# Performance work log

Measured on AMD Instinct MI355X. Metric: run time of the kernel, lower is better.

Reference implementation:

```python
import jax, jax.numpy as jnp
import numpy as np

B, MAX_T, S, H, NB, NA = 64, 511, 1024, 4096, 8, 4


def setup_inputs() -> dict:
    key = jax.random.key(0)
    k1, k2, k3, k4, k5 = jax.random.split(key, 5)
    s_i_batch = jax.random.normal(k1, (B, MAX_T + 1, S), dtype=jnp.float32)
    actions_batch = jax.random.randint(k2, (B, MAX_T), 0, NA, dtype=jnp.int32)
    lengths = jax.random.randint(k3, (B,), 0, MAX_T, dtype=jnp.int32)
    W1 = jax.random.normal(k4, (S, H), dtype=jnp.float32) * (1.0 / np.sqrt(S))
    b1 = jnp.zeros((H,), dtype=jnp.float32)
    W2 = jax.random.normal(k5, (H, NB * NA), dtype=jnp.float32) * (1.0 / np.sqrt(H))
    b2 = jnp.zeros((NB * NA,), dtype=jnp.float32)
    return {"s_i_batch": s_i_batch, "actions_batch": actions_batch,
            "lengths": lengths, "W1": W1, "b1": b1, "W2": W2, "b2": b2}


def reference(s_i_batch, actions_batch, lengths, W1, b1, W2, b2):
    Bc, Tp1, _ = s_i_batch.shape
    maxT = Tp1 - 1
    # control_net: MLP -> per-(option, action) log-probs
    h = jax.nn.relu(jnp.einsum('bts,sh->bth', s_i_batch, W1) + b1)
    logits = (jnp.einsum('bth,ha->bta', h, W2) + b2).reshape(Bc, Tp1, NB, NA)
    action_logps = jax.nn.log_softmax(logits, axis=-1)  # (B, T+1, b, 4)
    # option 0, timesteps 0..max_T-1
    lp0 = action_logps[:, :maxT, 0, :]                  # (B, max_T, 4)
    gathered = jnp.take_along_axis(lp0, actions_batch[..., None].astype(jnp.int32), axis=-1)[..., 0]
    mask = (jnp.arange(maxT)[None, :] < lengths[:, None]).astype(lp0.dtype)  # (B, max_T)
    total_logp = jnp.sum(gathered * mask)
    return -total_logp
```

## Files before the change

### kernel.cpp

```cpp
#include <hip/hip_runtime.h>
#include <hip/hip_bf16.h>
#include <math.h>

#define B_    64
#define MAXT  511
#define TP1   512
#define S_    1024
#define H_    4096
#define M_TOTAL (B_*TP1)
#define NITER (S_/32)

typedef __attribute__((ext_vector_type(8))) short  short8;
typedef __attribute__((ext_vector_type(4))) float  float4v;

#define ZBUF_BYTES ((size_t)M_TOTAL*4*sizeof(float))
#define SBF_OFF    0x81000
#define SBF_BYTES  ((size_t)M_TOTAL*S_*2)
#define W1T_OFF    (SBF_OFF + SBF_BYTES)

static __device__ __forceinline__ unsigned short f2bf(float f) {
    unsigned int u = __float_as_uint(f);
    u = u + 0x7fffu + ((u >> 16) & 1u);
    return (unsigned short)(u >> 16);
}

__global__ __launch_bounds__(256) void prep_kernel(const float* __restrict__ s,
                                                   const float* __restrict__ W1,
                                                   const int*   __restrict__ lengths,
                                                   unsigned short* __restrict__ Sb,
                                                   unsigned short* __restrict__ W1T) {
    int bid = blockIdx.x;
    if (bid < 16384) {
        int row = 2 * bid + (threadIdx.x >> 7);
        int b = row >> 9, t = row & 511;
        if (t >= lengths[b]) return;
        size_t idx = (size_t)row * S_ + (threadIdx.x & 127) * 8;
        float4v f0 = __builtin_nontemporal_load((const float4v*)(s + idx));
        float4v f1 = __builtin_nontemporal_load((const float4v*)(s + idx + 4));
        short8 o;
        o[0] = (short)f2bf(f0[0]); o[1] = (short)f2bf(f0[1]);
        o[2] = (short)f2bf(f0[2]); o[3] = (short)f2bf(f0[3]);
        o[4] = (short)f2bf(f1[0]); o[5] = (short)f2bf(f1[1]);
        o[6] = (short)f2bf(f1[2]); o[7] = (short)f2bf(f1[3]);
        *(short8*)(Sb + idx) = o;
    } else {
        __shared__ float tile[32][33];
        int tb = bid - 16384;
        int h0 = (tb & 127) * 32;
        int k0 = (tb >> 7) * 32;
        int tx = threadIdx.x & 31, ty = threadIdx.x >> 5;
        for (int r = ty; r < 32; r += 8)
            tile[r][tx] = __builtin_nontemporal_load(&W1[(size_t)(k0 + r) * H_ + h0 + tx]);
        __syncthreads();
        for (int r = ty; r < 32; r += 8)
            W1T[(size_t)(h0 + r) * S_ + k0 + tx] = f2bf(tile[tx][r]);
    }
}

__global__ __launch_bounds__(256) void gemm_fused_kernel(
        const unsigned short* __restrict__ Sb,
        const unsigned short* __restrict__ W1T,
        const float* __restrict__ b1,
        const float* __restrict__ W2,
        const int*   __restrict__ lengths,
        float*       __restrict__ zbuf)
{
    int id   = blockIdx.x;
    int xcd  = id & 7;
    int slot = id >> 3;
    int ntile = xcd * 4 + (slot & 3);
    int mtile = slot >> 2;

    int b  = mtile >> 2;
    int t0 = (mtile & 3) * 128;
    if (lengths[b] <= t0) return;

    int m0 = mtile * 128;
    int n0 = ntile * 128;

    __shared__ unsigned short smemA[2 * 128 * 32];
    __shared__ unsigned short smemB[2 * 128 * 32];

    int tid  = threadIdx.x;
    int wid  = tid >> 6;
    int lane = tid & 63;
    int lane15 = lane & 15;
    int quad   = lane >> 4;
    int wave_m = (wid >> 1) * 64;
    int wave_n = (wid & 1) * 64;

    int cA0 = tid, cA1 = tid + 256;
    int mA0 = cA0 >> 2, cp0 = cA0 & 3, q0 = cp0 ^ ((mA0 >> 1) & 3);
    int mA1 = cA1 >> 2, cp1 = cA1 & 3, q1 = cp1 ^ ((mA1 >> 1) & 3);

    const char* gA0 = (const char*)Sb  + (size_t)(m0 + mA0) * (S_*2) + q0 * 16;
    const char* gA1 = (const char*)Sb  + (size_t)(m0 + mA1) * (S_*2) + q1 * 16;
    const char* gB0 = (const char*)W1T + (size_t)(n0 + mA0) * (S_*2) + q0 * 16;
    const char* gB1 = (const char*)W1T + (size_t)(n0 + mA1) * (S_*2) + q1 * 16;
    char* lwA0 = (char*)smemA + cA0 * 16;
    char* lwA1 = (char*)smemA + cA1 * 16;
    char* lwB0 = (char*)smemB + cA0 * 16;
    char* lwB1 = (char*)smemB + cA1 * 16;

    int aOff[4], bOff[4];
#pragma unroll
    for (int s = 0; s < 4; s++) {
        int ml = wave_m + s * 16 + lane15;
        aOff[s] = ml * 32 + (quad ^ ((ml >> 1) & 3)) * 8;
        int nl = wave_n + s * 16 + lane15;
        bOff[s] = nl * 32 + (quad ^ ((nl >> 1) & 3)) * 8;
    }

    float4v acc[4][4] = {};
    short8 rA0[2], rA1[2], rB0[2], rB1[2];

    rA0[0] = *(const short8*)gA0; rA1[0] = *(const short8*)gA1;
    rB0[0] = *(const short8*)gB0; rB1[0] = *(const short8*)gB1;
    gA0 += 64; gA1 += 64; gB0 += 64; gB1 += 64;
    *(short8*)lwA0 = rA0[0]; *(short8*)lwA1 = rA1[0];
    *(short8*)lwB0 = rB0[0]; *(short8*)lwB1 = rB1[0];
    rA0[1] = *(const short8*)gA0; rA1[1] = *(const short8*)gA1;
    rB0[1] = *(const short8*)gB0; rB1[1] = *(const short8*)gB1;
    gA0 += 64; gA1 += 64; gB0 += 64; gB1 += 64;

    for (int k = 0; k < NITER; k += 2) {
        __syncthreads();
        if (k + 2 < NITER) {
            rA0[0] = *(const short8*)gA0; rA1[0] = *(const short8*)gA1;
            rB0[0] = *(const short8*)gB0; rB1[0] = *(const short8*)gB1;
            gA0 += 64; gA1 += 64; gB0 += 64; gB1 += 64;
        }
        *(short8*)(lwA0 + 8192) = rA0[1]; *(short8*)(lwA1 + 8192) = rA1[1];
        *(short8*)(lwB0 + 8192) = rB0[1]; *(short8*)(lwB1 + 8192) = rB1[1];
        {
            const unsigned short* aP = smemA;
            const unsigned short* bP = smemB;
            short8 af[4], bf[4];
#pragma unroll
            for (int s = 0; s < 4; s++) {
                af[s] = *(const short8*)(aP + aOff[s]);
                bf[s] = *(const short8*)(bP + bOff[s]);
            }
#pragma unroll
            for (int i = 0; i < 4; i++)
#pragma unroll
                for (int j = 0; j < 4; j++)
                    acc[i][j] = __builtin_amdgcn_mfma_f32_16x16x32_bf16(af[i], bf[j], acc[i][j], 0, 0, 0);
        }
        __syncthreads();
        if (k + 3 < NITER) {
            rA0[1] = *(const short8*)gA0; rA1[1] = *(const short8*)gA1;
            rB0[1] = *(const short8*)gB0; rB1[1] = *(const short8*)gB1;
            gA0 += 64; gA1 += 64; gB0 += 64; gB1 += 64;
        }
        if (k + 2 < NITER) {
            *(short8*)lwA0 = rA0[0]; *(short8*)lwA1 = rA1[0];
            *(short8*)lwB0 = rB0[0]; *(short8*)lwB1 = rB1[0];
        }
        {
            const unsigned short* aP = smemA + 4096;
            const unsigned short* bP = smemB + 4096;
            short8 af[4], bf[4];
#pragma unroll
            for (int s = 0; s < 4; s++) {
                af[s] = *(const short8*)(aP + aOff[s]);
                bf[s] = *(const short8*)(bP + bOff[s]);
            }
#pragma unroll
            for (int i = 0; i < 4; i++)
#pragma unroll
                for (int j = 0; j < 4; j++)
                    acc[i][j] = __builtin_amdgcn_mfma_f32_16x16x32_bf16(af[i], bf[j], acc[i][j], 0, 0, 0);
        }
    }

    float4v w2r[4];
    float   b1v[4];
#pragma unroll
    for (int ns = 0; ns < 4; ns++) {
        int n_g = n0 + wave_n + ns * 16 + lane15;
        w2r[ns] = *(const float4v*)(W2 + (size_t)n_g * 32);
        b1v[ns] = b1[n_g];
    }
#pragma unroll
    for (int ms = 0; ms < 4; ms++) {
        float p[4][4];
#pragma unroll
        for (int r = 0; r < 4; r++)
#pragma unroll
            for (int c = 0; c < 4; c++) p[r][c] = 0.f;
#pragma unroll
        for (int ns = 0; ns < 4; ns++) {
            float4v av = acc[ms][ns];
#pragma unroll
            for (int r = 0; r < 4; r++) {
                float h = av[r] + b1v[ns];
                h = h > 0.f ? h : 0.f;
                p[r][0] += h * w2r[ns][0];
                p[r][1] += h * w2r[ns][1];
                p[r][2] += h * w2r[ns][2];
                p[r][3] += h * w2r[ns][3];
            }
        }
#pragma unroll
        for (int off = 1; off < 16; off <<= 1)
#pragma unroll
            for (int r = 0; r < 4; r++)
#pragma unroll
                for (int c = 0; c < 4; c++)
                    p[r][c] += __shfl_xor(p[r][c], off);
        if (lane15 < 4) {
            int c = lane15;
#pragma unroll
            for (int r = 0; r < 4; r++) {
                int mg = m0 + wave_m + ms * 16 + quad * 4 + r;
                atomicAdd(&zbuf[(size_t)mg * 4 + c], p[r][c]);
            }
        }
    }
}

__global__ __launch_bounds__(128) void reduce_logp_kernel(
        const float* __restrict__ zbuf,
        const int*   __restrict__ actions,
        const int*   __restrict__ lengths,
        const float* __restrict__ b2,
        float*       __restrict__ out)
{
    int b = blockIdx.x;
    int t = blockIdx.y * 128 + threadIdx.x;
    int len = lengths[b];
    float local = 0.f;
    if (t < MAXT && t < len) {
        int row = b * TP1 + t;
        float4v z = *(const float4v*)(zbuf + (size_t)row * 4);
        float z0 = z[0] + b2[0], z1 = z[1] + b2[1], z2 = z[2] + b2[2], z3 = z[3] + b2[3];
        float mx = fmaxf(fmaxf(z0, z1), fmaxf(z2, z3));
        float se = expf(z0 - mx) + expf(z1 - mx) + expf(z2 - mx) + expf(z3 - mx);
        int a = actions[b * MAXT + t];
        float za = (a == 0) ? z0 : (a == 1) ? z1 : (a == 2) ? z2 : z3;
        local = (za - mx) - logf(se);
    }
#pragma unroll
    for (int off = 32; off > 0; off >>= 1) local += __shfl_xor(local, off);
    __shared__ float wsum[2];
    if ((threadIdx.x & 63) == 0) wsum[threadIdx.x >> 6] = local;
    __syncthreads();
    if (threadIdx.x == 0) atomicAdd(out, -(wsum[0] + wsum[1]));
}

extern "C" void kernel_launch(void* const* d_in, const int* in_sizes, int n_in,
                              void* d_out, int out_size, void* d_ws, size_t ws_size,
                              hipStream_t stream) {
    const float* s       = (const float*)d_in[0];
    const int*   actions = (const int*)  d_in[1];
    const int*   lengths = (const int*)  d_in[2];
    const float* W1      = (const float*)d_in[3];
    const float* b1      = (const float*)d_in[4];
    const float* W2      = (const float*)d_in[5];
    const float* b2      = (const float*)d_in[6];

    char* ws = (char*)d_ws;
    float*          zbuf = (float*)ws;
    unsigned short* Sb   = (unsigned short*)(ws + SBF_OFF);
    unsigned short* W1T  = (unsigned short*)(ws + W1T_OFF);

    hipMemsetAsync(ws, 0, ZBUF_BYTES, stream);
    hipMemsetAsync(d_out, 0, sizeof(float), stream);

    prep_kernel<<<dim3(16384 + 4096), 256, 0, stream>>>(s, W1, lengths, Sb, W1T);
    gemm_fused_kernel<<<dim3(8192), 256, 0, stream>>>(Sb, W1T, b1, W2, lengths, zbuf);
    reduce_logp_kernel<<<dim3(B_, 4), 128, 0, stream>>>(zbuf, actions, lengths, b2, (float*)d_out);
}
```

Before: 525.6 us.

## Use 512-thread GEMM blocks with 8 waves and widen W1 transpose tiles

The fused GEMM kernel moves from 4 waves with 64x64 tiles each to 8 waves with 64x32 tiles each over the same 128x128 block tile. Each thread now loads one 16-byte chunk per operand per stage, which cuts per-thread registers and raises the number of waves that can hide latency, at the cost of more LDS fragment reads per MFMA. The W1 transpose in the prep kernel switches to 64x64 tiles with float4 loads and 4-element bf16 stores, reducing block count and making memory accesses wider. The epilogue cross-lane reduction and the atomic updates now run across twice as many waves.

```diff
diff --git a/kernel.cpp b/kernel.cpp
--- a/kernel.cpp
+++ b/kernel.cpp
@@ -11,6 +11,7 @@
 #define NITER (S_/32)
 
 typedef __attribute__((ext_vector_type(8))) short  short8;
+typedef __attribute__((ext_vector_type(4))) short  short4v;
 typedef __attribute__((ext_vector_type(4))) float  float4v;
 
 #define ZBUF_BYTES ((size_t)M_TOTAL*4*sizeof(float))
@@ -44,20 +45,33 @@
         o[6] = (short)f2bf(f1[2]); o[7] = (short)f2bf(f1[3]);
         *(short8*)(Sb + idx) = o;
     } else {
-        __shared__ float tile[32][33];
+        __shared__ float tile[64][65];
         int tb = bid - 16384;
-        int h0 = (tb & 127) * 32;
-        int k0 = (tb >> 7) * 32;
-        int tx = threadIdx.x & 31, ty = threadIdx.x >> 5;
-        for (int r = ty; r < 32; r += 8)
-            tile[r][tx] = __builtin_nontemporal_load(&W1[(size_t)(k0 + r) * H_ + h0 + tx]);
+        int h0 = (tb & 63) * 64;
+        int k0 = (tb >> 6) * 64;
+        int fx = threadIdx.x & 15;
+        int r  = threadIdx.x >> 4;
+        for (int rr = r; rr < 64; rr += 16) {
+            float4v v = __builtin_nontemporal_load(
+                (const float4v*)(W1 + (size_t)(k0 + rr) * H_ + h0 + fx * 4));
+            tile[rr][fx*4+0] = v[0]; tile[rr][fx*4+1] = v[1];
+            tile[rr][fx*4+2] = v[2]; tile[rr][fx*4+3] = v[3];
+        }
         __syncthreads();
-        for (int r = ty; r < 32; r += 8)
-            W1T[(size_t)(h0 + r) * S_ + k0 + tx] = f2bf(tile[tx][r]);
-    }
-}
-
-__global__ __launch_bounds__(256) void gemm_fused_kernel(
+        int c4 = threadIdx.x & 15;
+        int hr = threadIdx.x >> 4;
+        for (int hh = hr; hh < 64; hh += 16) {
+            short4v o;
+            o[0] = (short)f2bf(tile[c4*4+0][hh]);
+            o[1] = (short)f2bf(tile[c4*4+1][hh]);
+            o[2] = (short)f2bf(tile[c4*4+2][hh]);
+            o[3] = (short)f2bf(tile[c4*4+3][hh]);
+            *(short4v*)(W1T + (size_t)(h0 + hh) * S_ + k0 + c4 * 4) = o;
+        }
+    }
+}
+
+__global__ __launch_bounds__(512, 4) void gemm_fused_kernel(
         const unsigned short* __restrict__ Sb,
         const unsigned short* __restrict__ W1T,
         const float* __restrict__ b1,
@@ -86,98 +100,82 @@
     int lane = tid & 63;
     int lane15 = lane & 15;
     int quad   = lane >> 4;
-    int wave_m = (wid >> 1) * 64;
-    int wave_n = (wid & 1) * 64;
-
-    int cA0 = tid, cA1 = tid + 256;
-    int mA0 = cA0 >> 2, cp0 = cA0 & 3, q0 = cp0 ^ ((mA0 >> 1) & 3);
-    int mA1 = cA1 >> 2, cp1 = cA1 & 3, q1 = cp1 ^ ((mA1 >> 1) & 3);
-
-    const char* gA0 = (const char*)Sb  + (size_t)(m0 + mA0) * (S_*2) + q0 * 16;
-    const char* gA1 = (const char*)Sb  + (size_t)(m0 + mA1) * (S_*2) + q1 * 16;
-    const char* gB0 = (const char*)W1T + (size_t)(n0 + mA0) * (S_*2) + q0 * 16;
-    const char* gB1 = (const char*)W1T + (size_t)(n0 + mA1) * (S_*2) + q1 * 16;
-    char* lwA0 = (char*)smemA + cA0 * 16;
-    char* lwA1 = (char*)smemA + cA1 * 16;
-    char* lwB0 = (char*)smemB + cA0 * 16;
-    char* lwB1 = (char*)smemB + cA1 * 16;
-
-    int aOff[4], bOff[4];
+    int wave_m = (wid >> 2) * 64;
+    int wave_n = (wid & 3) * 32;
+
+    int mA = tid >> 2, cp = tid & 3, q = cp ^ ((mA >> 1) & 3);
+
+    const char* gA = (const char*)Sb  + (size_t)(m0 + mA) * (S_*2) + q * 16;
+    const char* gB = (const char*)W1T + (size_t)(n0 + mA) * (S_*2) + q * 16;
+    char* lwA = (char*)smemA + tid * 16;
+    char* lwB = (char*)smemB + tid * 16;
+
+    int aOff[4], bOff[2];
 #pragma unroll
     for (int s = 0; s < 4; s++) {
         int ml = wave_m + s * 16 + lane15;
         aOff[s] = ml * 32 + (quad ^ ((ml >> 1) & 3)) * 8;
+    }
+#pragma unroll
+    for (int s = 0; s < 2; s++) {
         int nl = wave_n + s * 16 + lane15;
         bOff[s] = nl * 32 + (quad ^ ((nl >> 1) & 3)) * 8;
     }
 
-    float4v acc[4][4] = {};
-    short8 rA0[2], rA1[2], rB0[2], rB1[2];
-
-    rA0[0] = *(const short8*)gA0; rA1[0] = *(const short8*)gA1;
-    rB0[0] = *(const short8*)gB0; rB1[0] = *(const short8*)gB1;
-    gA0 += 64; gA1 += 64; gB0 += 64; gB1 += 64;
-    *(short8*)lwA0 = rA0[0]; *(short8*)lwA1 = rA1[0];
-    *(short8*)lwB0 = rB0[0]; *(short8*)lwB1 = rB1[0];
-    rA0[1] = *(const short8*)gA0; rA1[1] = *(const short8*)gA1;
-    rB0[1] = *(const short8*)gB0; rB1[1] = *(const short8*)gB1;
-    gA0 += 64; gA1 += 64; gB0 += 64; gB1 += 64;
+    float4v acc[4][2] = {};
+    short8 rA[2], rB[2];
+
+    rA[0] = *(const short8*)(gA);        rB[0] = *(const short8*)(gB);
+    rA[1] = *(const short8*)(gA + 64);   rB[1] = *(const short8*)(gB + 64);
+    *(short8*)lwA = rA[0]; *(short8*)lwB = rB[0];
+    rA[0] = *(const short8*)(gA + 128);  rB[0] = *(const short8*)(gB + 128);
 
     for (int k = 0; k < NITER; k += 2) {
         __syncthreads();
+        *(short8*)(lwA + 8192) = rA[1]; *(short8*)(lwB + 8192) = rB[1];
+        if (k + 3 < NITER) {
+            rA[1] = *(const short8*)(gA + 192);
+            rB[1] = *(const short8*)(gB + 192);
+        }
+        {
+            short8 af[4], bf[2];
+#pragma unroll
+            for (int s = 0; s < 4; s++) af[s] = *(const short8*)(smemA + aOff[s]);
+#pragma unroll
+            for (int s = 0; s < 2; s++) bf[s] = *(const short8*)(smemB + bOff[s]);
+#pragma unroll
+            for (int i = 0; i < 4; i++)
+#pragma unroll
+                for (int j = 0; j < 2; j++)
+                    acc[i][j] = __builtin_amdgcn_mfma_f32_16x16x32_bf16(af[i], bf[j], acc[i][j], 0, 0, 0);
+        }
+        __syncthreads();
         if (k + 2 < NITER) {
-            rA0[0] = *(const short8*)gA0; rA1[0] = *(const short8*)gA1;
-            rB0[0] = *(const short8*)gB0; rB1[0] = *(const short8*)gB1;
-            gA0 += 64; gA1 += 64; gB0 += 64; gB1 += 64;
-        }
-        *(short8*)(lwA0 + 8192) = rA0[1]; *(short8*)(lwA1 + 8192) = rA1[1];
-        *(short8*)(lwB0 + 8192) = rB0[1]; *(short8*)(lwB1 + 8192) = rB1[1];
+            *(short8*)lwA = rA[0]; *(short8*)lwB = rB[0];
+        }
+        if (k + 4 < NITER) {
+            rA[0] = *(const short8*)(gA + 256);
+            rB[0] = *(const short8*)(gB + 256);
+        }
+        gA += 128; gB += 128;
         {
-            const unsigned short* aP = smemA;
-            const unsigned short* bP = smemB;
-            short8 af[4], bf[4];
-#pragma unroll
-            for (int s = 0; s < 4; s++) {
-                af[s] = *(const short8*)(aP + aOff[s]);
-                bf[s] = *(const short8*)(bP + bOff[s]);
-            }
+            short8 af[4], bf[2];
+#pragma unroll
+            for (int s = 0; s < 4; s++) af[s] = *(const short8*)(smemA + 4096 + aOff[s]);
+#pragma unroll
+            for (int s = 0; s < 2; s++) bf[s] = *(const short8*)(smemB + 4096 + bOff[s]);
 #pragma unroll
             for (int i = 0; i < 4; i++)
 #pragma unroll
-                for (int j = 0; j < 4; j++)
+                for (int j = 0; j < 2; j++)
                     acc[i][j] = __builtin_amdgcn_mfma_f32_16x16x32_bf16(af[i], bf[j], acc[i][j], 0, 0, 0);
         }
-        __syncthreads();
-        if (k + 3 < NITER) {
-            rA0[1] = *(const short8*)gA0; rA1[1] = *(const short8*)gA1;
-            rB0[1] = *(const short8*)gB0; rB1[1] = *(const short8*)gB1;
-            gA0 += 64; gA1 += 64; gB0 += 64; gB1 += 64;
-        }
-        if (k + 2 < NITER) {
-            *(short8*)lwA0 = rA0[0]; *(short8*)lwA1 = rA1[0];
-            *(short8*)lwB0 = rB0[0]; *(short8*)lwB1 = rB1[0];
-        }
-        {
-            const unsigned short* aP = smemA + 4096;
-            const unsigned short* bP = smemB + 4096;
-            short8 af[4], bf[4];
-#pragma unroll
-            for (int s = 0; s < 4; s++) {
-                af[s] = *(const short8*)(aP + aOff[s]);
-                bf[s] = *(const short8*)(bP + bOff[s]);
-            }
-#pragma unroll
-            for (int i = 0; i < 4; i++)
-#pragma unroll
-                for (int j = 0; j < 4; j++)
-                    acc[i][j] = __builtin_amdgcn_mfma_f32_16x16x32_bf16(af[i], bf[j], acc[i][j], 0, 0, 0);
-        }
-    }
-
-    float4v w2r[4];
-    float   b1v[4];
-#pragma unroll
-    for (int ns = 0; ns < 4; ns++) {
+    }
+
+    float4v w2r[2];
+    float   b1v[2];
+#pragma unroll
+    for (int ns = 0; ns < 2; ns++) {
         int n_g = n0 + wave_n + ns * 16 + lane15;
         w2r[ns] = *(const float4v*)(W2 + (size_t)n_g * 32);
         b1v[ns] = b1[n_g];
@@ -190,7 +188,7 @@
 #pragma unroll
             for (int c = 0; c < 4; c++) p[r][c] = 0.f;
 #pragma unroll
-        for (int ns = 0; ns < 4; ns++) {
+        for (int ns = 0; ns < 2; ns++) {
             float4v av = acc[ms][ns];
 #pragma unroll
             for (int r = 0; r < 4; r++) {
@@ -268,7 +266,7 @@
     hipMemsetAsync(ws, 0, ZBUF_BYTES, stream);
     hipMemsetAsync(d_out, 0, sizeof(float), stream);
 
-    prep_kernel<<<dim3(16384 + 4096), 256, 0, stream>>>(s, W1, lengths, Sb, W1T);
-    gemm_fused_kernel<<<dim3(8192), 256, 0, stream>>>(Sb, W1T, b1, W2, lengths, zbuf);
+    prep_kernel<<<dim3(16384 + 1024), 256, 0, stream>>>(s, W1, lengths, Sb, W1T);
+    gemm_fused_kernel<<<dim3(8192), 512, 0, stream>>>(Sb, W1T, b1, W2, lengths, zbuf);
     reduce_logp_kernel<<<dim3(B_, 4), 128, 0, stream>>>(zbuf, actions, lengths, b2, (float*)d_out);
 }
```

Result: slower. 669.9 us (+27.4%).
